# Optimization experiments

Hardware: AMD Instinct MI355X
Metric: run time of the kernel (lower is better)

The kernel has to match this reference:

```python
import jax, jax.numpy as jnp
import numpy as np

N = 100000      # nodes
E = 3200000     # edges (avg degree 32)
FEA = 67
HID = 16
OUT = 2
K = 3           # num_stacks
T = 2           # num_layers


def setup_inputs() -> dict:
    key = jax.random.key(0)
    ks = jax.random.split(key, 11)
    s = 0.1  # weight init scale
    return {
        "x": jax.random.normal(ks[0], (N, FEA), jnp.float32),
        "edge_index": jax.random.randint(ks[1], (2, E), 0, N, dtype=jnp.int32),
        "init_w1": jax.random.normal(ks[2], (K, FEA, HID), jnp.float32) * s,
        "w1": jax.random.normal(ks[3], (1, K, HID, HID), jnp.float32) * s,
        "root_w1": jax.random.normal(ks[4], (1, K, FEA, HID), jnp.float32) * s,
        "b1": jax.random.normal(ks[5], (1, K, 1, HID), jnp.float32) * s,
        "init_w2": jax.random.normal(ks[6], (K, HID, OUT), jnp.float32) * s,
        "w2": jax.random.normal(ks[7], (1, K, OUT, OUT), jnp.float32) * s,
        "root_w2": jax.random.normal(ks[8], (1, K, HID, OUT), jnp.float32) * s,
        "b2": jax.random.normal(ks[9], (1, K, 1, OUT), jnp.float32) * s,
    }


def gcn_norm(src, dst, n):
    # symmetric normalization of A WITHOUT self-loops (PyG ARMAConv behavior)
    deg = jax.ops.segment_sum(jnp.ones(src.shape[0], jnp.float32), dst, num_segments=n)
    dinv = jnp.where(deg > 0, jax.lax.rsqrt(jnp.maximum(deg, 1.0)), 0.0)
    return dinv[src] * dinv[dst]  # [E]


def arma_conv(x, src, dst, norm, init_w, w, root_w, bias, act, n):
    # x: [N, Fin]; shared_weights=True, num_layers=T, num_stacks=K
    out = jnp.einsum('nf,kfh->knh', x, init_w)           # t=0 transform
    root = jnp.einsum('nf,kfh->knh', x, root_w[0])       # root term (dropout=identity in eval)
    for t in range(T):
        if t > 0:
            out = jnp.einsum('knh,khp->knp', out, w[0])
        # propagate: out[i] = sum_{(j->i)} norm_e * out[j]
        m = (out[:, src, :] * norm[None, :, None]).transpose(1, 0, 2)  # [E,K,H]
        agg = jax.ops.segment_sum(m, dst, num_segments=n).transpose(1, 0, 2)  # [K,N,H]
        out = agg + root + bias[0]
        if act:
            out = jax.nn.relu(out)
    return out.mean(axis=0)  # average over stacks -> [N, H]


def reference(x, edge_index, init_w1, w1, root_w1, b1, init_w2, w2, root_w2, b2):
    src, dst = edge_index[0], edge_index[1]
    n = x.shape[0]
    norm = gcn_norm(src, dst, n)
    h = jax.nn.relu(arma_conv(x, src, dst, norm, init_w1, w1, root_w1, b1, True, n))
    o = arma_conv(h, src, dst, norm, init_w2, w2, root_w2, b2, False, n)
    return jax.nn.log_softmax(o, axis=1)
```

## Files before the change

### kernel.cpp

```cpp
#include <hip/hip_runtime.h>
#include <hip/hip_fp16.h>
#include <math.h>

#define NN 100000
#define NE 3200000
#define FEA 67
#define HID 16
#define OUTC 2
#define KS 3
#define KH 48
#define KO 6
#define PAD 64

#define PB 512
#define EPB 6250
#define BINW 512
#define NBINS 196
#define M1 (NBINS * PB)
#define NSCB 98


__global__ void k_hist(const int* __restrict__ dst, int* __restrict__ hist) {
    __shared__ int h[NBINS];
    if (threadIdx.x < NBINS) h[threadIdx.x] = 0;
    __syncthreads();
    int base = blockIdx.x * EPB;
    for (int i = threadIdx.x; i < EPB; i += 256)
        atomicAdd(&h[dst[base + i] >> 9], 1);
    __syncthreads();
    if (threadIdx.x < NBINS) hist[threadIdx.x * PB + blockIdx.x] = h[threadIdx.x];
}


__global__ void k_partial(const int* __restrict__ in, int* __restrict__ partials, int n) {
    __shared__ int s[256];
    int base = blockIdx.x * 1024;
    int acc = 0;
    for (int i = threadIdx.x; i < 1024; i += 256) {
        int idx = base + i;
        if (idx < n) acc += in[idx];
    }
    s[threadIdx.x] = acc;
    __syncthreads();
    for (int off = 128; off > 0; off >>= 1) {
        if (threadIdx.x < off) s[threadIdx.x] += s[threadIdx.x + off];
        __syncthreads();
    }
    if (threadIdx.x == 0) partials[blockIdx.x] = s[0];
}

__global__ void k_downsweepF(const int* __restrict__ in, const int* __restrict__ partials,
                             int* __restrict__ out, int n) {
    __shared__ int ps[256];
    __shared__ int s[256];
    int t = threadIdx.x;
    ps[t] = (t < NSCB) ? partials[t] : 0;
    __syncthreads();
    for (int off = 1; off < 256; off <<= 1) {
        int v = (t >= off) ? ps[t - off] : 0;
        __syncthreads();
        ps[t] += v;
        __syncthreads();
    }
    int bbase = (blockIdx.x > 0) ? ps[blockIdx.x - 1] : 0;

    int base = blockIdx.x * 1024 + t * 4;
    int d0 = 0, d1 = 0, d2 = 0, d3 = 0;
    if (base + 0 < n) d0 = in[base + 0];
    if (base + 1 < n) d1 = in[base + 1];
    if (base + 2 < n) d2 = in[base + 2];
    if (base + 3 < n) d3 = in[base + 3];
    int ts = d0 + d1 + d2 + d3;
    s[t] = ts;
    __syncthreads();
    for (int off = 1; off < 256; off <<= 1) {
        int v = (t >= off) ? s[t - off] : 0;
        __syncthreads();
        s[t] += v;
        __syncthreads();
    }
    int excl = s[t] - ts + bbase;
    if (base + 0 < n) out[base + 0] = excl;
    if (base + 1 < n) out[base + 1] = excl + d0;
    if (base + 2 < n) out[base + 2] = excl + d0 + d1;
    if (base + 3 < n) out[base + 3] = excl + d0 + d1 + d2;
}


__global__ void k_pass2(const int* __restrict__ src, const int* __restrict__ dst,
                        const int* __restrict__ hist_scan, int* __restrict__ recs) {
    __shared__ int curs[NBINS];
    if (threadIdx.x < NBINS) curs[threadIdx.x] = hist_scan[threadIdx.x * PB + blockIdx.x];
    __syncthreads();
    int base = blockIdx.x * EPB;
    for (int i = threadIdx.x; i < EPB; i += 256) {
        int e = base + i;
        int s = src[e], d = dst[e];
        int pos = atomicAdd(&curs[d >> 9], 1);
        recs[pos] = s | ((d & 511) << 17);
    }
}


__global__ void k_degsort(const int* __restrict__ recs, const int* __restrict__ hist_scan,
                          int* __restrict__ deg, float* __restrict__ dinv,
                          int* __restrict__ row_start, int* __restrict__ csr) {
    __shared__ int cnt[BINW];
    __shared__ int scn[BINW];
    int bin = blockIdx.x, t = threadIdx.x;
    cnt[t] = 0;
    __syncthreads();
    int s0 = hist_scan[bin * PB];
    int s1 = (bin + 1 < NBINS) ? hist_scan[(bin + 1) * PB] : NE;
    for (int r = s0 + t; r < s1; r += BINW)
        atomicAdd(&cnt[((unsigned)recs[r]) >> 17], 1);
    __syncthreads();
    scn[t] = cnt[t];
    __syncthreads();
    for (int off = 1; off < BINW; off <<= 1) {
        int v = (t >= off) ? scn[t - off] : 0;
        __syncthreads();
        scn[t] += v;
        __syncthreads();
    }
    int node = bin * BINW + t;
    int rs = s0 + scn[t] - cnt[t];
    if (node < NN) {
        int c = cnt[t];
        deg[node]       = c;
        dinv[node]      = (c > 0) ? rsqrtf((float)c) : 0.f;
        row_start[node] = rs;
    }
    scn[t] = rs;
    __syncthreads();
    for (int r = s0 + t; r < s1; r += BINW) {
        int rec = recs[r];
        int pos = atomicAdd(&scn[((unsigned)rec) >> 17], 1);
        csr[pos] = rec & 0x1FFFF;
    }
}


__global__ void k_transform1(const float* __restrict__ x, const float* __restrict__ iw,
                             const float* __restrict__ rw, const float* __restrict__ b1,
                             const float* __restrict__ dinv,
                             __half* __restrict__ A, __half* __restrict__ Bpad,
                             float* __restrict__ R) {
    if (blockIdx.x == NN / 16) {
        int t = threadIdx.x;
        if (t < PAD) A[(size_t)NN * PAD + t] = __float2half(0.f);
        else if (t < 2 * PAD) Bpad[(size_t)NN * PAD + (t - PAD)] = __float2half(0.f);
        return;
    }
    __shared__ float xs[16 * FEA];
    __shared__ float w0[KS * FEA * HID];
    __shared__ float wr[KS * FEA * HID];
    __shared__ float bb[KH];
    int n0 = blockIdx.x * 16;
    for (int i = threadIdx.x; i < KS * FEA * HID; i += 256) { w0[i] = iw[i]; wr[i] = rw[i]; }
    if (threadIdx.x < KH) bb[threadIdx.x] = b1[threadIdx.x];
    for (int i = threadIdx.x; i < 16 * FEA; i += 256) xs[i] = x[n0 * FEA + i];
    __syncthreads();
    for (int it = threadIdx.x; it < 16 * 24; it += 256) {
        int nl = it / 24, m = it % 24;
        int j0 = 2 * m;
        int k = j0 >> 4, h0 = j0 & 15;
        const float* wp0 = &w0[k * FEA * HID + h0];
        const float* wpr = &wr[k * FEA * HID + h0];
        const float* xp  = &xs[nl * FEA];
        float a0 = 0.f, a1 = 0.f, r0 = bb[j0], r1 = bb[j0 + 1];
        #pragma unroll
        for (int f = 0; f < FEA; ++f) {
            float xv = xp[f];
            a0 += xv * wp0[f * HID];
            a1 += xv * wp0[f * HID + 1];
            r0 += xv * wpr[f * HID];
            r1 += xv * wpr[f * HID + 1];
        }
        int n = n0 + nl;
        float dvn = dinv[n];
        ((__half2*)A)[(size_t)n * (PAD / 2) + m] =
            __halves2half2(__float2half_rn(a0 * dvn), __float2half_rn(a1 * dvn));
        *(float2*)&R[(size_t)n * KH + j0] = make_float2(r0, r1);
    }
}


template <bool FUSEW>
__global__ void k_spmm48(const __half2* __restrict__ Asrc,
                         const float* __restrict__ R,
                         const int* __restrict__ row_start, const int* __restrict__ deg,
                         const float* __restrict__ dinv, const int* __restrict__ csr,
                         const float* __restrict__ w1, __half2* __restrict__ Bout) {
    __shared__ float w1s[FUSEW ? KS * HID * HID : 1];
    if (FUSEW) {
        for (int i = threadIdx.x; i < KS * HID * HID; i += 256) w1s[i] = w1[i];
        __syncthreads();
    }
    int node = (blockIdx.x * 256 + threadIdx.x) >> 6;
    int lane = threadIdx.x & 63;
    int eo   = lane >> 5;
    int cl   = lane & 31;
    int start = __builtin_amdgcn_readfirstlane(row_start[node]);
    int d     = __builtin_amdgcn_readfirstlane(deg[node]);
    float dv  = dinv[node];
    float ax = 0.f, ay = 0.f;
    for (int b = 0; b < d; b += 64) {
        int nb  = min(64, d - b);
        int myc = csr[start + b + lane];
        int npf = nb >> 1;
        int p = 0;
        for (; p + 4 <= npf; p += 4) {
            int c0 = __shfl(myc, 2 * (p + 0) + eo, 64);
            int c1 = __shfl(myc, 2 * (p + 1) + eo, 64);
            int c2 = __shfl(myc, 2 * (p + 2) + eo, 64);
            int c3 = __shfl(myc, 2 * (p + 3) + eo, 64);
            float2 f0 = __half22float2(Asrc[(size_t)c0 * (PAD / 2) + cl]);
            float2 f1 = __half22float2(Asrc[(size_t)c1 * (PAD / 2) + cl]);
            float2 f2 = __half22float2(Asrc[(size_t)c2 * (PAD / 2) + cl]);
            float2 f3 = __half22float2(Asrc[(size_t)c3 * (PAD / 2) + cl]);
            ax += f0.x + f1.x; ay += f0.y + f1.y;
            ax += f2.x + f3.x; ay += f2.y + f3.y;
        }
        for (; p < npf; ++p) {
            int c = __shfl(myc, 2 * p + eo, 64);
            float2 f = __half22float2(Asrc[(size_t)c * (PAD / 2) + cl]);
            ax += f.x; ay += f.y;
        }
        if (nb & 1) {
            int c = __shfl(myc, nb - 1, 64);
            c = (eo == 0) ? c : NN;
            float2 f = __half22float2(Asrc[(size_t)c * (PAD / 2) + cl]);
            ax += f.x; ay += f.y;
        }
    }
    ax += __shfl_xor(ax, 32, 64);
    ay += __shfl_xor(ay, 32, 64);
    float2 r2 = make_float2(0.f, 0.f);
    if (cl < 24) r2 = *(const float2*)&R[(size_t)node * KH + 2 * cl];
    float vx = fmaxf(ax * dv + r2.x, 0.f);
    float vy = fmaxf(ay * dv + r2.y, 0.f);
    if (FUSEW) {
        int k  = cl >> 3;
        int p0 = (2 * cl) & 15;
        float o0 = 0.f, o1 = 0.f;
        #pragma unroll
        for (int h2 = 0; h2 < 8; ++h2) {
            float ix = __shfl(vx, k * 8 + h2, 64);
            float iy = __shfl(vy, k * 8 + h2, 64);
            o0 += ix * w1s[k * 256 + (2 * h2) * 16 + p0]     + iy * w1s[k * 256 + (2 * h2 + 1) * 16 + p0];
            o1 += ix * w1s[k * 256 + (2 * h2) * 16 + p0 + 1] + iy * w1s[k * 256 + (2 * h2 + 1) * 16 + p0 + 1];
        }
        if (eo == 0 && cl < 24)
            Bout[(size_t)node * (PAD / 2) + cl] =
                __halves2half2(__float2half_rn(o0 * dv), __float2half_rn(o1 * dv));
    } else {
        if (eo == 0 && cl < 24)
            Bout[(size_t)node * (PAD / 2) + cl] =
                __halves2half2(__float2half_rn(vx), __float2half_rn(vy));
    }
}


__global__ void k_mt2(const __half* __restrict__ L1, const float* __restrict__ iw,
                      const float* __restrict__ rw, const float* __restrict__ b2,
                      const float* __restrict__ dinv,
                      float* __restrict__ A2, float* __restrict__ R2) {
    __shared__ float wi[KS * HID * OUTC];
    __shared__ float wr_[KS * HID * OUTC];
    __shared__ float bb[KO];
    if (threadIdx.x < KS * HID * OUTC) { wi[threadIdx.x] = iw[threadIdx.x]; wr_[threadIdx.x] = rw[threadIdx.x]; }
    if (threadIdx.x < KO) bb[threadIdx.x] = b2[threadIdx.x];
    __syncthreads();
    int n = blockIdx.x * 256 + threadIdx.x;
    if (n >= NN) return;
    const __half2* hp = (const __half2*)(L1 + (size_t)n * PAD);
    float v[KH];
    #pragma unroll
    for (int q = 0; q < 24; ++q) {
        float2 f = __half22float2(hp[q]);
        v[q * 2 + 0] = f.x; v[q * 2 + 1] = f.y;
    }
    float h[HID];
    #pragma unroll
    for (int hh = 0; hh < HID; ++hh)
        h[hh] = fmaxf((v[hh] + v[16 + hh] + v[32 + hh]) * (1.f / 3.f), 0.f);
    float dv = dinv[n];
    #pragma unroll
    for (int k = 0; k < KS; ++k) {
        #pragma unroll
        for (int o = 0; o < OUTC; ++o) {
            float a = 0.f, r = bb[k * 2 + o];
            #pragma unroll
            for (int hh = 0; hh < HID; ++hh) {
                a += h[hh] * wi[k * 32 + hh * 2 + o];
                r += h[hh] * wr_[k * 32 + hh * 2 + o];
            }
            A2[n * KO + k * 2 + o] = a * dv;
            R2[n * KO + k * 2 + o] = r;
        }
    }
}


__global__ void k_spmm6_g(const float* __restrict__ Asrc, const float* __restrict__ R2,
                          const int* __restrict__ row_start, const int* __restrict__ deg,
                          const float* __restrict__ dinv, const int* __restrict__ csr,
                          const float* __restrict__ w2, float* __restrict__ Bout) {
    __shared__ float ws[KS * OUTC * OUTC];
    if (threadIdx.x < KS * OUTC * OUTC) ws[threadIdx.x] = w2[threadIdx.x];
    __syncthreads();
    int t = blockIdx.x * 256 + threadIdx.x;
    int node = t / KO, j = t % KO;
    bool active = node < NN;
    float acc = 0.f, r = 0.f, dv = 0.f;
    int start = 0, d = 0;
    if (active) {
        start = row_start[node];
        d     = deg[node];
        r     = R2[node * KO + j];
        dv    = dinv[node];
    }
    int e = 0;
    for (; e + 4 <= d; e += 4) {
        int c0 = csr[start + e + 0];
        int c1 = csr[start + e + 1];
        int c2 = csr[start + e + 2];
        int c3 = csr[start + e + 3];
        acc += Asrc[c0 * KO + j];
        acc += Asrc[c1 * KO + j];
        acc += Asrc[c2 * KO + j];
        acc += Asrc[c3 * KO + j];
    }
    for (; e < d; ++e)
        acc += Asrc[csr[start + e] * KO + j];
    float v = acc * dv + r;
    float other = __shfl_xor(v, 1, 64);
    if (active) {
        int k = j >> 1, p = j & 1;
        float v0 = (p == 0) ? v : other;
        float v1 = (p == 0) ? other : v;
        Bout[node * KO + j] = (v0 * ws[k * 4 + p] + v1 * ws[k * 4 + 2 + p]) * dv;
    }
}


__global__ void k_spmm6_f(const float* __restrict__ Asrc, const float* __restrict__ R2,
                          const int* __restrict__ row_start, const int* __restrict__ deg,
                          const float* __restrict__ dinv, const int* __restrict__ csr,
                          float* __restrict__ out) {
    int wave = threadIdx.x >> 6;
    int l    = threadIdx.x & 63;
    int nl   = l / 6;
    int j    = l - nl * 6;
    bool active = nl < 10;
    int node = blockIdx.x * 40 + wave * 10 + nl;
    float acc = 0.f, r = 0.f, dv = 0.f;
    int start = 0, d = 0;
    if (active) {
        start = row_start[node];
        d     = deg[node];
        r     = R2[node * KO + j];
        dv    = dinv[node];
    }
    int e = 0;
    for (; e + 4 <= d; e += 4) {
        int c0 = csr[start + e + 0];
        int c1 = csr[start + e + 1];
        int c2 = csr[start + e + 2];
        int c3 = csr[start + e + 3];
        acc += Asrc[c0 * KO + j];
        acc += Asrc[c1 * KO + j];
        acc += Asrc[c2 * KO + j];
        acc += Asrc[c3 * KO + j];
    }
    for (; e < d; ++e)
        acc += Asrc[csr[start + e] * KO + j];
    float v = acc * dv + r;
    int base = nl * 6;
    float o0 = (__shfl(v, base + 0, 64) + __shfl(v, base + 2, 64) + __shfl(v, base + 4, 64)) * (1.f / 3.f);
    float o1 = (__shfl(v, base + 1, 64) + __shfl(v, base + 3, 64) + __shfl(v, base + 5, 64)) * (1.f / 3.f);
    if (active && j == 0) {
        float m = fmaxf(o0, o1);
        float ls = m + logf(expf(o0 - m) + expf(o1 - m));
        *(float2*)(out + (size_t)node * 2) = make_float2(o0 - ls, o1 - ls);
    }
}


extern "C" void kernel_launch(void* const* d_in, const int* in_sizes, int n_in,
                              void* d_out, int out_size, void* d_ws, size_t ws_size,
                              hipStream_t stream) {
    const float* x   = (const float*)d_in[0];
    const int*   ei  = (const int*)d_in[1];
    const float* iw1 = (const float*)d_in[2];
    const float* w1  = (const float*)d_in[3];
    const float* rw1 = (const float*)d_in[4];
    const float* b1  = (const float*)d_in[5];
    const float* iw2 = (const float*)d_in[6];
    const float* w2  = (const float*)d_in[7];
    const float* rw2 = (const float*)d_in[8];
    const float* b2  = (const float*)d_in[9];
    const int* src = ei;
    const int* dst = ei + NE;
    float* out = (float*)d_out;

    char* ws = (char*)d_ws;
    size_t o = 0;
    int*    deg       = (int*)(ws + o);    o += (size_t)NN * 4;
    int*    row_start = (int*)(ws + o);    o += (size_t)NN * 4;
    float*  dinv      = (float*)(ws + o);  o += (size_t)NN * 4;
    int*    hist      = (int*)(ws + o);    o += (size_t)M1 * 4;
    int*    hist_scan = (int*)(ws + o);    o += (size_t)M1 * 4;
    int*    partials  = (int*)(ws + o);    o += 128 * 4;
    int*    csr       = (int*)(ws + o);    o += (size_t)(NE + 64) * 4;
    __half* A         = (__half*)(ws + o); o += (size_t)(NN + 1) * PAD * 2;
    float*  R         = (float*)(ws + o);  o += (size_t)NN * KH * 4;
    __half* B         = (__half*)(ws + o); o += (size_t)(NN + 1) * PAD * 2;
    int*    recs  = (int*)A;
    __half* L1f   = A;
    float*  A2    = R;
    float*  R2    = R + (size_t)NN * KO;
    float*  C2    = R + (size_t)NN * KO * 2;

    k_hist       <<<PB, 256, 0, stream>>>(dst, hist);
    k_partial    <<<NSCB, 256, 0, stream>>>(hist, partials, M1);
    k_downsweepF <<<NSCB, 256, 0, stream>>>(hist, partials, hist_scan, M1);
    k_pass2      <<<PB, 256, 0, stream>>>(src, dst, hist_scan, recs);
    k_degsort    <<<NBINS, BINW, 0, stream>>>(recs, hist_scan, deg, dinv, row_start, csr);

    k_transform1    <<<NN / 16 + 1, 256, 0, stream>>>(x, iw1, rw1, b1, dinv, A, B, R);
    k_spmm48<true>  <<<NN / 4, 256, 0, stream>>>((const __half2*)A, R, row_start, deg, dinv, csr, w1, (__half2*)B);
    k_spmm48<false> <<<NN / 4, 256, 0, stream>>>((const __half2*)B, R, row_start, deg, dinv, csr, w1, (__half2*)L1f);

    k_mt2      <<<(NN + 255) / 256, 256, 0, stream>>>(L1f, iw2, rw2, b2, dinv, A2, R2);
    k_spmm6_g  <<<(NN * KO + 255) / 256, 256, 0, stream>>>(A2, R2, row_start, deg, dinv, csr, w2, C2);
    k_spmm6_f  <<<NN / 40, 256, 0, stream>>>(C2, R2, row_start, deg, dinv, csr, out);
}
```

Measured before the change: 344.1 us.

## Register-tile the first dense transform with 128-node blocks and transposed smem weights

Rewrites the x·W transform kernel to process 128 nodes per block instead of 16. Each thread computes a 4-node by 12-output register tile from transposed, padded shared-memory copies of x and the weights, using float4 loads. The old kernel reloaded about 26 KB of weights into shared memory for every 16 nodes. The new one amortizes that load over eight times more nodes and cuts shared-memory traffic per FMA. It costs higher register pressure (48 accumulators) and a strided transposed load of x into shared memory.

```diff
diff --git a/kernel.cpp b/kernel.cpp
--- a/kernel.cpp
+++ b/kernel.cpp
@@ -19,6 +19,11 @@
 #define M1 (NBINS * PB)
 #define NSCB 98
 
+#define TBM 128
+#define TNB ((NN + TBM - 1) / TBM)
+#define XS_STRIDE 132
+#define WT_STRIDE 68
+
 
 __global__ void k_hist(const int* __restrict__ dst, int* __restrict__ hist) {
     __shared__ int h[NBINS];
@@ -146,42 +151,97 @@
                              const float* __restrict__ dinv,
                              __half* __restrict__ A, __half* __restrict__ Bpad,
                              float* __restrict__ R) {
-    if (blockIdx.x == NN / 16) {
+    if (blockIdx.x == TNB) {
         int t = threadIdx.x;
         if (t < PAD) A[(size_t)NN * PAD + t] = __float2half(0.f);
         else if (t < 2 * PAD) Bpad[(size_t)NN * PAD + (t - PAD)] = __float2half(0.f);
         return;
     }
-    __shared__ float xs[16 * FEA];
-    __shared__ float w0[KS * FEA * HID];
-    __shared__ float wr[KS * FEA * HID];
+    __shared__ float xs[FEA * XS_STRIDE];
+    __shared__ float wTs[96 * WT_STRIDE];
     __shared__ float bb[KH];
-    int n0 = blockIdx.x * 16;
-    for (int i = threadIdx.x; i < KS * FEA * HID; i += 256) { w0[i] = iw[i]; wr[i] = rw[i]; }
+    int n0g = blockIdx.x * TBM;
+
+    for (int idx = threadIdx.x; idx < 96 * FEA; idx += 256) {
+        int j = idx / FEA, f = idx % FEA;
+        float v;
+        if (j < KH) v = iw[(j >> 4) * (FEA * HID) + f * HID + (j & 15)];
+        else { int jr = j - KH; v = rw[(jr >> 4) * (FEA * HID) + f * HID + (jr & 15)]; }
+        wTs[j * WT_STRIDE + f] = v;
+    }
     if (threadIdx.x < KH) bb[threadIdx.x] = b1[threadIdx.x];
-    for (int i = threadIdx.x; i < 16 * FEA; i += 256) xs[i] = x[n0 * FEA + i];
-    __syncthreads();
-    for (int it = threadIdx.x; it < 16 * 24; it += 256) {
-        int nl = it / 24, m = it % 24;
-        int j0 = 2 * m;
-        int k = j0 >> 4, h0 = j0 & 15;
-        const float* wp0 = &w0[k * FEA * HID + h0];
-        const float* wpr = &wr[k * FEA * HID + h0];
-        const float* xp  = &xs[nl * FEA];
-        float a0 = 0.f, a1 = 0.f, r0 = bb[j0], r1 = bb[j0 + 1];
-        #pragma unroll
-        for (int f = 0; f < FEA; ++f) {
-            float xv = xp[f];
-            a0 += xv * wp0[f * HID];
-            a1 += xv * wp0[f * HID + 1];
-            r0 += xv * wpr[f * HID];
-            r1 += xv * wpr[f * HID + 1];
-        }
-        int n = n0 + nl;
-        float dvn = dinv[n];
-        ((__half2*)A)[(size_t)n * (PAD / 2) + m] =
-            __halves2half2(__float2half_rn(a0 * dvn), __float2half_rn(a1 * dvn));
-        *(float2*)&R[(size_t)n * KH + j0] = make_float2(r0, r1);
+    for (int idx = threadIdx.x; idx < TBM * FEA; idx += 256) {
+        int nl = idx / FEA, f = idx % FEA;
+        int n = n0g + nl;
+        xs[f * XS_STRIDE + nl] = (n < NN) ? x[(size_t)n * FEA + f] : 0.f;
+    }
+    __syncthreads();
+
+    int tx = threadIdx.x & 31, ty = threadIdx.x >> 5;
+    int nl0 = tx * 4;
+    int j0  = ty * 12;
+    float acc[4][12];
+    #pragma unroll
+    for (int p = 0; p < 12; ++p) {
+        float init = (j0 >= KH) ? bb[j0 - KH + p] : 0.f;
+        acc[0][p] = init; acc[1][p] = init; acc[2][p] = init; acc[3][p] = init;
+    }
+
+    #pragma unroll 4
+    for (int fb = 0; fb < 16; ++fb) {
+        int f0 = fb * 4;
+        float4 xv0 = *(const float4*)&xs[(f0 + 0) * XS_STRIDE + nl0];
+        float4 xv1 = *(const float4*)&xs[(f0 + 1) * XS_STRIDE + nl0];
+        float4 xv2 = *(const float4*)&xs[(f0 + 2) * XS_STRIDE + nl0];
+        float4 xv3 = *(const float4*)&xs[(f0 + 3) * XS_STRIDE + nl0];
+        #pragma unroll
+        for (int p = 0; p < 12; ++p) {
+            float4 wv = *(const float4*)&wTs[(j0 + p) * WT_STRIDE + f0];
+            acc[0][p] += xv0.x * wv.x + xv1.x * wv.y + xv2.x * wv.z + xv3.x * wv.w;
+            acc[1][p] += xv0.y * wv.x + xv1.y * wv.y + xv2.y * wv.z + xv3.y * wv.w;
+            acc[2][p] += xv0.z * wv.x + xv1.z * wv.y + xv2.z * wv.z + xv3.z * wv.w;
+            acc[3][p] += xv0.w * wv.x + xv1.w * wv.y + xv2.w * wv.z + xv3.w * wv.w;
+        }
+    }
+    #pragma unroll
+    for (int f = 64; f < FEA; ++f) {
+        float x0 = xs[f * XS_STRIDE + nl0 + 0];
+        float x1 = xs[f * XS_STRIDE + nl0 + 1];
+        float x2 = xs[f * XS_STRIDE + nl0 + 2];
+        float x3 = xs[f * XS_STRIDE + nl0 + 3];
+        #pragma unroll
+        for (int p = 0; p < 12; ++p) {
+            float wv = wTs[(j0 + p) * WT_STRIDE + f];
+            acc[0][p] += x0 * wv; acc[1][p] += x1 * wv;
+            acc[2][p] += x2 * wv; acc[3][p] += x3 * wv;
+        }
+    }
+
+    if (j0 < KH) {
+        #pragma unroll
+        for (int nq = 0; nq < 4; ++nq) {
+            int n = n0g + nl0 + nq;
+            if (n < NN) {
+                float dv = dinv[n];
+                __half2* Ap = (__half2*)A + (size_t)n * (PAD / 2) + (j0 >> 1);
+                #pragma unroll
+                for (int p2 = 0; p2 < 6; ++p2)
+                    Ap[p2] = __halves2half2(__float2half_rn(acc[nq][2 * p2] * dv),
+                                            __float2half_rn(acc[nq][2 * p2 + 1] * dv));
+            }
+        }
+    } else {
+        int jr = j0 - KH;
+        #pragma unroll
+        for (int nq = 0; nq < 4; ++nq) {
+            int n = n0g + nl0 + nq;
+            if (n < NN) {
+                float* Rp = &R[(size_t)n * KH + jr];
+                *(float4*)(Rp + 0) = make_float4(acc[nq][0], acc[nq][1], acc[nq][2],  acc[nq][3]);
+                *(float4*)(Rp + 4) = make_float4(acc[nq][4], acc[nq][5], acc[nq][6],  acc[nq][7]);
+                *(float4*)(Rp + 8) = make_float4(acc[nq][8], acc[nq][9], acc[nq][10], acc[nq][11]);
+            }
+        }
     }
 }
 
@@ -429,7 +489,7 @@
     k_pass2      <<<PB, 256, 0, stream>>>(src, dst, hist_scan, recs);
     k_degsort    <<<NBINS, BINW, 0, stream>>>(recs, hist_scan, deg, dinv, row_start, csr);
 
-    k_transform1    <<<NN / 16 + 1, 256, 0, stream>>>(x, iw1, rw1, b1, dinv, A, B, R);
+    k_transform1    <<<TNB + 1, 256, 0, stream>>>(x, iw1, rw1, b1, dinv, A, B, R);
     k_spmm48<true>  <<<NN / 4, 256, 0, stream>>>((const __half2*)A, R, row_start, deg, dinv, csr, w1, (__half2*)B);
     k_spmm48<false> <<<NN / 4, 256, 0, stream>>>((const __half2*)B, R, row_start, deg, dinv, csr, w1, (__half2*)L1f);
 
```

Measured after the change: 330.8 us. -3.9%, faster.
